# Kernel tuning notes

Hardware: AMD Instinct MI355X
Metric: run time of the kernel (lower is better)

Reference implementation:

```python
import jax, jax.numpy as jnp
import numpy as np

# Grid constants (ERA5 0.25deg source -> 1deg destination)
N_A = 721 * 1440      # 1,038,240 source cells
N_B = 181 * 360       # 65,160 destination cells
NY, NX = 181, 360     # dst_shape (reshape_to_xy=True)
NNZ = 4 * N_B         # ~4 bilinear weights per destination cell
FLIP_AXIS = (-2,)


def setup_inputs() -> dict:
    key = jax.random.key(0)
    k1, k2, k3, k4 = jax.random.split(key, 4)
    x = jax.random.normal(k1, (2, 70, 721, 1440), dtype=jnp.float32)
    rows = jax.random.randint(k2, (NNZ,), 0, N_B, dtype=jnp.int64)
    cols = jax.random.randint(k3, (NNZ,), 0, N_A, dtype=jnp.int64)
    weights = jax.random.uniform(k4, (NNZ,), dtype=jnp.float32)
    return {"x": x, "rows": rows, "cols": cols, "weights": weights}


def reference(x, rows, cols, weights):
    # flip_axis=[-2]: flip latitude axis of source grid
    x = jnp.flip(x, axis=FLIP_AXIS)
    lead_shape = x.shape[:-2]
    # flatten spatial dims: (N, n_a) where N = prod(lead_shape)
    x_flat = x.reshape(-1, N_A)
    # sparse mm W @ x_flat.T as gather + weighted segment-sum:
    # gathered[n, k] = weights[k] * x_flat[n, cols[k]]   -> (N, nnz)
    gathered = x_flat[:, cols] * weights
    # y_flat[b, n] = sum_{k: rows[k]==b} gathered[n, k]  -> (N, n_b)
    y_flat = jax.ops.segment_sum(gathered.T, rows, num_segments=N_B).T
    # reshape_to_xy=True with dst_shape = (NY, NX)
    return y_flat.reshape(*lead_shape, NY, NX)
```

## Files before the change

### kernel.cpp

```cpp
#include <hip/hip_runtime.h>
#include <hip/hip_fp16.h>


#define NXS 1440
#define NYS 721
#define N_A_CONST (721 * 1440)
#define N_B_CONST (181 * 360)
#define NBUCKC ((N_A_CONST + 63) / 64)
#define NFIELD 140
#define NPAIR (NFIELD / 2)
#define GDW 72
#define TILE 16384

__device__ __forceinline__ int flip_col(int c) {
    int iy = c / NXS;
    int ix = c - iy * NXS;
    return (NYS - 1 - iy) * NXS + ix;
}


__global__ void zero_ws_kernel(int* __restrict__ p, int n) {
    int i = blockIdx.x * blockDim.x + threadIdx.x;
    int stride = gridDim.x * blockDim.x;
    for (; i < n; i += stride) p[i] = 0;
}

__global__ void hist2_kernel(const int* __restrict__ rows, const int* __restrict__ cols,
                             int* __restrict__ bcount, int* __restrict__ rcount, int nnz) {
    int k = blockIdx.x * blockDim.x + threadIdx.x;
    if (k >= nnz) return;
    int cf = flip_col(cols[k]);
    atomicAdd(&bcount[cf >> 6], 1);
    atomicAdd(&rcount[rows[k]], 1);
}

__global__ __launch_bounds__(1024)
void scan_lds_kernel(const int* __restrict__ bcount, int* __restrict__ boff,
                     const int* __restrict__ rcount, int* __restrict__ roff) {
    __shared__ int tile[TILE];
    __shared__ int wsum[16];
    __shared__ int carry_s;
    const int* in; int* out; int n;
    if (blockIdx.x == 0) { in = bcount; out = boff; n = NBUCKC; }
    else                 { in = rcount; out = roff; n = N_B_CONST; }
    int t = threadIdx.x;
    int lane = t & 63, wv = t >> 6;
    if (t == 0) carry_s = 0;
    __syncthreads();

    for (int base = 0; base < n; base += TILE) {
        #pragma unroll
        for (int i = 0; i < 16; ++i) {
            int idx = base + i * 1024 + t;
            tile[i * 1024 + t] = (idx < n) ? in[idx] : 0;
        }
        __syncthreads();
        int s = 0;
        #pragma unroll
        for (int i = 0; i < 16; ++i) s += tile[t * 16 + i];

        int incl = s;
        #pragma unroll
        for (int off = 1; off < 64; off <<= 1) {
            int u = __shfl_up(incl, off, 64);
            if (lane >= off) incl += u;
        }
        if (lane == 63) wsum[wv] = incl;
        __syncthreads();
        if (t < 16) {
            int v = wsum[t];
            #pragma unroll
            for (int off = 1; off < 16; off <<= 1) {
                int u = __shfl_up(v, off, 16);
                if (t >= off) v += u;
            }
            wsum[t] = v;
        }
        __syncthreads();
        int waveoff = (wv == 0) ? 0 : wsum[wv - 1];
        int carry = carry_s;
        int run = carry + waveoff + incl - s;
        #pragma unroll
        for (int i = 0; i < 16; ++i) {
            int old = tile[t * 16 + i];
            tile[t * 16 + i] = run;
            run += old;
        }
        __syncthreads();
        if (t == 1023) carry_s = run;
        #pragma unroll
        for (int i = 0; i < 16; ++i) {
            int idx = base + i * 1024 + t;
            if (idx < n) out[idx] = tile[i * 1024 + t];
        }
        __syncthreads();
    }
    if (t == 0) out[n] = carry_s;
}

__global__ void perm2_kernel(const int* __restrict__ rows, const int* __restrict__ cols,
                             const float* __restrict__ w,
                             const int* __restrict__ boff, int* __restrict__ bcur,
                             const int* __restrict__ roff, int* __restrict__ rcur,
                             int4* __restrict__ perm, int nnz) {
    int k = blockIdx.x * blockDim.x + threadIdx.x;
    if (k >= nnz) return;
    int cf = flip_col(cols[k]);
    int bu = cf >> 6;
    int j_cf = boff[bu] + atomicAdd(&bcur[bu], 1);
    int b = rows[k];
    int j_row = roff[b] + atomicAdd(&rcur[b], 1);
    perm[j_cf] = make_int4(cf, __float_as_int(w[k]), j_row, 0);
}


__global__ __launch_bounds__(256, 2)
void gather_kernel(const float* __restrict__ x, const int4* __restrict__ perm,
                   unsigned int* __restrict__ g, int nnz) {
    int j = blockIdx.x * 256 + (int)threadIdx.x;
    bool act = j < nnz;
    int4 p = perm[act ? j : (nnz - 1)];
    const float* xp = x + p.x;
    float wj = __int_as_float(p.y);

    unsigned int v[NPAIR];
    #pragma unroll
    for (int pp = 0; pp < NPAIR; ++pp) {
        float f0 = xp[(size_t)(2 * pp) * N_A_CONST];
        float f1 = xp[(size_t)(2 * pp + 1) * N_A_CONST];
        unsigned int lo = __half_as_ushort(__float2half(wj * f0));
        unsigned int hi = __half_as_ushort(__float2half(wj * f1));
        v[pp] = lo | (hi << 16);
    }

    if (act) {
        uint4* gp = (uint4*)(g + (size_t)p.z * GDW);
        #pragma unroll
        for (int i = 0; i < 17; ++i)
            gp[i] = make_uint4(v[4 * i], v[4 * i + 1], v[4 * i + 2], v[4 * i + 3]);
        gp[17] = make_uint4(v[68], v[69], 0u, 0u);
    }
}

__device__ __forceinline__ float h2f_lo(unsigned int d) {
    return __half2float(__ushort_as_half((unsigned short)(d & 0xffffu)));
}
__device__ __forceinline__ float h2f_hi(unsigned int d) {
    return __half2float(__ushort_as_half((unsigned short)(d >> 16)));
}

__global__ __launch_bounds__(256)
void reduce_kernel(const unsigned int* __restrict__ g, const int* __restrict__ roff,
                   float* __restrict__ out) {
    __shared__ float lds[64][141];
    int b0 = blockIdx.x * 64;
    int lane = threadIdx.x & 63;
    int wv = threadIdx.x >> 6;

    for (int i = 0; i < 16; ++i) {
        int bl = wv * 16 + i;
        int b = b0 + bl;
        if (b < N_B_CONST) {
            int p0 = roff[b], p1 = roff[b + 1];
            float a0 = 0.f, a1 = 0.f, a2 = 0.f, a3 = 0.f;
            for (int pos = p0; pos < p1; ++pos) {
                const unsigned int* gr = g + (size_t)pos * GDW;
                unsigned int d = gr[lane];
                a0 += h2f_lo(d); a1 += h2f_hi(d);
                if (lane < 6) {
                    unsigned int e = gr[64 + lane];
                    a2 += h2f_lo(e); a3 += h2f_hi(e);
                }
            }
            lds[bl][2 * lane]     = a0;
            lds[bl][2 * lane + 1] = a1;
            if (lane < 6) {
                lds[bl][128 + 2 * lane] = a2;
                lds[bl][129 + 2 * lane] = a3;
            }
        }
    }
    __syncthreads();

    int nb = N_B_CONST - b0; if (nb > 64) nb = 64;
    for (int idx = threadIdx.x; idx < NFIELD * 64; idx += 256) {
        int f = idx >> 6;
        int rr = idx & 63;
        if (rr < nb)
            out[(size_t)f * N_B_CONST + b0 + rr] = lds[rr][f];
    }
}


__global__ void zero_out_kernel(float* __restrict__ out, int n) {
    int i = blockIdx.x * blockDim.x + threadIdx.x;
    int stride = gridDim.x * blockDim.x;
    for (; i < n; i += stride) out[i] = 0.0f;
}

__global__ void scatter_fallback_kernel(const float* __restrict__ x, const int* __restrict__ rows,
                                        const int* __restrict__ cols, const float* __restrict__ w,
                                        float* __restrict__ out, int nnz) {
    int k = blockIdx.x * blockDim.x + threadIdx.x;
    if (k >= nnz) return;
    int n = blockIdx.y;
    int cf = flip_col(cols[k]);
    float v = w[k] * x[(size_t)n * N_A_CONST + cf];
    atomicAdd(out + (size_t)n * N_B_CONST + rows[k], v);
}

extern "C" void kernel_launch(void* const* d_in, const int* in_sizes, int n_in,
                              void* d_out, int out_size, void* d_ws, size_t ws_size,
                              hipStream_t stream) {
    const float* x    = (const float*)d_in[0];
    const int*   rows = (const int*)d_in[1];
    const int*   cols = (const int*)d_in[2];
    const float* w    = (const float*)d_in[3];
    float* out = (float*)d_out;

    int nnz    = in_sizes[1];
    int nfield = in_sizes[0] / N_A_CONST;

    size_t o = 0;
    size_t bcount_o = o; o += NBUCKC;
    size_t bcur_o   = o; o += NBUCKC;
    size_t rcount_o = o; o += N_B_CONST;
    size_t rcur_o   = o; o += N_B_CONST;
    size_t zero_span = o;
    size_t boff_o   = o; o += NBUCKC + 1;
    size_t roff_o   = o; o += N_B_CONST + 1;
    o = (o + 31) & ~(size_t)31;
    size_t perm_o   = o; o += 4 * (size_t)nnz;
    o = (o + 31) & ~(size_t)31;
    size_t g_o      = o;
    size_t need_bytes = (g_o + (size_t)nnz * GDW) * sizeof(int);

    if (ws_size < need_bytes || nfield != NFIELD) {
        zero_out_kernel<<<2048, 256, 0, stream>>>(out, out_size);
        dim3 grid((nnz + 255) / 256, nfield);
        scatter_fallback_kernel<<<grid, 256, 0, stream>>>(x, rows, cols, w, out, nnz);
        return;
    }

    int*  wsI    = (int*)d_ws;
    int*  bcount = wsI + bcount_o;
    int*  bcur   = wsI + bcur_o;
    int*  rcount = wsI + rcount_o;
    int*  rcur   = wsI + rcur_o;
    int*  boff   = wsI + boff_o;
    int*  roff   = wsI + roff_o;
    int4* perm   = (int4*)(wsI + perm_o);
    unsigned int* g = (unsigned int*)(wsI + g_o);

    zero_ws_kernel<<<512, 256, 0, stream>>>(wsI, (int)zero_span);

    int nblk = (nnz + 255) / 256;
    hist2_kernel<<<nblk, 256, 0, stream>>>(rows, cols, bcount, rcount, nnz);
    scan_lds_kernel<<<2, 1024, 0, stream>>>(bcount, boff, rcount, roff);
    perm2_kernel<<<nblk, 256, 0, stream>>>(rows, cols, w, boff, bcur, roff, rcur, perm, nnz);

    gather_kernel<<<nblk, 256, 0, stream>>>(x, perm, g, nnz);

    int rblk = (N_B_CONST + 63) / 64;
    reduce_kernel<<<rblk, 256, 0, stream>>>(g, roff, out);
}
```

Baseline: 295.8 us.

## Gather by dense 128-cell source windows with coalesced loads and wave shuffles

Source cells are now bucketed into 128-cell windows instead of 64-cell buckets. Each wavefront owns one window: every lane loads two adjacent cells per field as a coalesced float2, and each nonzero picks its value from the owning lane with a wave shuffle. This replaces scattered per-nonzero loads across 140 strided fields with streaming reads of x. The cost is reading the whole source array even though only about a quarter of the cells are referenced. Windows with more than 64 entries fall back to the old per-entry scattered gather.

```diff
diff --git a/kernel.cpp b/kernel.cpp
--- a/kernel.cpp
+++ b/kernel.cpp
@@ -6,7 +6,8 @@
 #define NYS 721
 #define N_A_CONST (721 * 1440)
 #define N_B_CONST (181 * 360)
-#define NBUCKC ((N_A_CONST + 63) / 64)
+#define WF 128
+#define NWIN ((N_A_CONST + WF - 1) / WF)
 #define NFIELD 140
 #define NPAIR (NFIELD / 2)
 #define GDW 72
@@ -26,22 +27,22 @@
 }
 
 __global__ void hist2_kernel(const int* __restrict__ rows, const int* __restrict__ cols,
-                             int* __restrict__ bcount, int* __restrict__ rcount, int nnz) {
+                             int* __restrict__ wcount, int* __restrict__ rcount, int nnz) {
     int k = blockIdx.x * blockDim.x + threadIdx.x;
     if (k >= nnz) return;
     int cf = flip_col(cols[k]);
-    atomicAdd(&bcount[cf >> 6], 1);
+    atomicAdd(&wcount[cf >> 7], 1);
     atomicAdd(&rcount[rows[k]], 1);
 }
 
 __global__ __launch_bounds__(1024)
-void scan_lds_kernel(const int* __restrict__ bcount, int* __restrict__ boff,
+void scan_lds_kernel(const int* __restrict__ wcount, int* __restrict__ woff,
                      const int* __restrict__ rcount, int* __restrict__ roff) {
     __shared__ int tile[TILE];
     __shared__ int wsum[16];
     __shared__ int carry_s;
     const int* in; int* out; int n;
-    if (blockIdx.x == 0) { in = bcount; out = boff; n = NBUCKC; }
+    if (blockIdx.x == 0) { in = wcount; out = woff; n = NWIN; }
     else                 { in = rcount; out = roff; n = N_B_CONST; }
     int t = threadIdx.x;
     int lane = t & 63, wv = t >> 6;
@@ -100,14 +101,14 @@
 
 __global__ void perm2_kernel(const int* __restrict__ rows, const int* __restrict__ cols,
                              const float* __restrict__ w,
-                             const int* __restrict__ boff, int* __restrict__ bcur,
+                             const int* __restrict__ woff, int* __restrict__ wcur,
                              const int* __restrict__ roff, int* __restrict__ rcur,
                              int4* __restrict__ perm, int nnz) {
     int k = blockIdx.x * blockDim.x + threadIdx.x;
     if (k >= nnz) return;
     int cf = flip_col(cols[k]);
-    int bu = cf >> 6;
-    int j_cf = boff[bu] + atomicAdd(&bcur[bu], 1);
+    int wu = cf >> 7;
+    int j_cf = woff[wu] + atomicAdd(&wcur[wu], 1);
     int b = rows[k];
     int j_row = roff[b] + atomicAdd(&rcur[b], 1);
     perm[j_cf] = make_int4(cf, __float_as_int(w[k]), j_row, 0);
@@ -116,25 +117,62 @@
 
 __global__ __launch_bounds__(256, 2)
 void gather_kernel(const float* __restrict__ x, const int4* __restrict__ perm,
-                   unsigned int* __restrict__ g, int nnz) {
-    int j = blockIdx.x * 256 + (int)threadIdx.x;
-    bool act = j < nnz;
-    int4 p = perm[act ? j : (nnz - 1)];
-    const float* xp = x + p.x;
+                   const int* __restrict__ woff, unsigned int* __restrict__ g) {
+    int wid = blockIdx.x * 4 + ((int)threadIdx.x >> 6);
+    int lane = (int)threadIdx.x & 63;
+    if (wid >= NWIN) return;
+    int base = wid * WF;
+    int j0 = woff[wid], j1 = woff[wid + 1];
+    int count = j1 - j0;
+    if (count == 0) return;
+
+    bool act = lane < count;
+    int4 p = perm[act ? (j0 + lane) : j0];
+    int o = p.x - base;
+    int src = o >> 1, comp = o & 1;
     float wj = __int_as_float(p.y);
+
+    int i2 = base + 2 * lane;
+    bool ldok = (i2 + 1) < N_A_CONST;
 
     unsigned int v[NPAIR];
     #pragma unroll
     for (int pp = 0; pp < NPAIR; ++pp) {
-        float f0 = xp[(size_t)(2 * pp) * N_A_CONST];
-        float f1 = xp[(size_t)(2 * pp + 1) * N_A_CONST];
-        unsigned int lo = __half_as_ushort(__float2half(wj * f0));
-        unsigned int hi = __half_as_ushort(__float2half(wj * f1));
+        float2 xa = ldok ? *(const float2*)&x[(size_t)(2 * pp) * N_A_CONST + i2]
+                         : make_float2(0.f, 0.f);
+        float2 xb = ldok ? *(const float2*)&x[(size_t)(2 * pp + 1) * N_A_CONST + i2]
+                         : make_float2(0.f, 0.f);
+        float a0 = __shfl(xa.x, src, 64);
+        float a1 = __shfl(xa.y, src, 64);
+        float b0 = __shfl(xb.x, src, 64);
+        float b1 = __shfl(xb.y, src, 64);
+        float fa = comp ? a1 : a0;
+        float fb = comp ? b1 : b0;
+        unsigned int lo = __half_as_ushort(__float2half(wj * fa));
+        unsigned int hi = __half_as_ushort(__float2half(wj * fb));
         v[pp] = lo | (hi << 16);
     }
 
     if (act) {
         uint4* gp = (uint4*)(g + (size_t)p.z * GDW);
+        #pragma unroll
+        for (int i = 0; i < 17; ++i)
+            gp[i] = make_uint4(v[4 * i], v[4 * i + 1], v[4 * i + 2], v[4 * i + 3]);
+        gp[17] = make_uint4(v[68], v[69], 0u, 0u);
+    }
+
+    for (int jj = j0 + 64 + lane; jj < j1; jj += 64) {
+        int4 q = perm[jj];
+        const float* xp = x + q.x;
+        float qw = __int_as_float(q.y);
+        #pragma unroll
+        for (int pp = 0; pp < NPAIR; ++pp) {
+            float f0 = xp[(size_t)(2 * pp) * N_A_CONST];
+            float f1 = xp[(size_t)(2 * pp + 1) * N_A_CONST];
+            v[pp] = __half_as_ushort(__float2half(qw * f0)) |
+                    ((unsigned int)__half_as_ushort(__float2half(qw * f1)) << 16);
+        }
+        uint4* gp = (uint4*)(g + (size_t)q.z * GDW);
         #pragma unroll
         for (int i = 0; i < 17; ++i)
             gp[i] = make_uint4(v[4 * i], v[4 * i + 1], v[4 * i + 2], v[4 * i + 3]);
@@ -222,12 +260,12 @@
     int nfield = in_sizes[0] / N_A_CONST;
 
     size_t o = 0;
-    size_t bcount_o = o; o += NBUCKC;
-    size_t bcur_o   = o; o += NBUCKC;
+    size_t wcount_o = o; o += NWIN;
+    size_t wcur_o   = o; o += NWIN;
     size_t rcount_o = o; o += N_B_CONST;
     size_t rcur_o   = o; o += N_B_CONST;
     size_t zero_span = o;
-    size_t boff_o   = o; o += NBUCKC + 1;
+    size_t woff_o   = o; o += NWIN + 1;
     size_t roff_o   = o; o += N_B_CONST + 1;
     o = (o + 31) & ~(size_t)31;
     size_t perm_o   = o; o += 4 * (size_t)nnz;
@@ -243,11 +281,11 @@
     }
 
     int*  wsI    = (int*)d_ws;
-    int*  bcount = wsI + bcount_o;
-    int*  bcur   = wsI + bcur_o;
+    int*  wcount = wsI + wcount_o;
+    int*  wcur   = wsI + wcur_o;
     int*  rcount = wsI + rcount_o;
     int*  rcur   = wsI + rcur_o;
-    int*  boff   = wsI + boff_o;
+    int*  woff   = wsI + woff_o;
     int*  roff   = wsI + roff_o;
     int4* perm   = (int4*)(wsI + perm_o);
     unsigned int* g = (unsigned int*)(wsI + g_o);
@@ -255,11 +293,12 @@
     zero_ws_kernel<<<512, 256, 0, stream>>>(wsI, (int)zero_span);
 
     int nblk = (nnz + 255) / 256;
-    hist2_kernel<<<nblk, 256, 0, stream>>>(rows, cols, bcount, rcount, nnz);
-    scan_lds_kernel<<<2, 1024, 0, stream>>>(bcount, boff, rcount, roff);
-    perm2_kernel<<<nblk, 256, 0, stream>>>(rows, cols, w, boff, bcur, roff, rcur, perm, nnz);
-
-    gather_kernel<<<nblk, 256, 0, stream>>>(x, perm, g, nnz);
+    hist2_kernel<<<nblk, 256, 0, stream>>>(rows, cols, wcount, rcount, nnz);
+    scan_lds_kernel<<<2, 1024, 0, stream>>>(wcount, woff, rcount, roff);
+    perm2_kernel<<<nblk, 256, 0, stream>>>(rows, cols, w, woff, wcur, roff, rcur, perm, nnz);
+
+    int gblk = (NWIN + 3) / 4;
+    gather_kernel<<<gblk, 256, 0, stream>>>(x, perm, woff, g);
 
     int rblk = (N_B_CONST + 63) / 64;
     reduce_kernel<<<rblk, 256, 0, stream>>>(g, roff, out);
```

Result: slower. 379.6 us (+28.3%).
